# Performance work log

Hardware: AMD Instinct MI355X
Metric: run time of the kernel (lower is better)

## Reference

```python
import jax, jax.numpy as jnp
import numpy as np

B = 4096       # batch
N_IN = 784     # input neurons
BANKS = 64     # banks per layer
L = 16         # layers of banks (layer 0 = input banks)
FAN = 8        # fan-out per source bank into next layer
D = 10         # n_neurons_per_hidd_bank
N_CONN = (L - 1) * BANKS * FAN  # total bank connections (7680)


def setup_inputs() -> dict:
    key = jax.random.key(0)
    ks = jax.random.split(key, 7)
    x = jax.random.normal(ks[0], (B, N_IN), jnp.float32)
    # input2hidden: Linear(N_IN, D, bias=True) for each input bank -> weight [D, N_IN]
    Wi = jax.random.normal(ks[1], (BANKS, D, N_IN), jnp.float32) / np.sqrt(N_IN).astype(np.float32)
    bi = jax.random.normal(ks[2], (BANKS, D), jnp.float32) * 0.1
    # per-edge gate: Linear(D, 1, bias=True); bias shifted so gates are a mix of open/closed
    Wg = jax.random.normal(ks[3], (L - 1, BANKS, FAN, D), jnp.float32) / np.sqrt(D).astype(np.float32)
    bg = jax.random.normal(ks[4], (L - 1, BANKS, FAN), jnp.float32) * 0.3 + 0.2
    # per-edge data: Linear(D, D, bias=False) -> weight [out=D, in=D]
    Wd = jax.random.normal(ks[5], (L - 1, BANKS, FAN, D, D), jnp.float32) / np.sqrt(D).astype(np.float32)
    # hidden2output: Linear(D, 1, bias=False) per output bank
    Wo = jax.random.normal(ks[6], (BANKS, D), jnp.float32) / np.sqrt(D).astype(np.float32)
    return {"x": x, "Wi": Wi, "bi": bi, "Wg": Wg, "bg": bg, "Wd": Wd, "Wo": Wo}


def reference(x, Wi, bi, Wg, bg, Wd, Wo):
    # forward_softgate with defaults: no batch norm, dropout p=0 (identity),
    # gates enabled (b_no_gates=False), positive gate loss, no gate_status.
    batch = x.shape[0]
    # static scatter targets: source bank s feeds banks (s+k)%BANKS of next layer
    s = np.arange(BANKS)[:, None]
    k = np.arange(FAN)[None, :]
    tgt = jnp.asarray(((s + k) % BANKS).reshape(-1))  # [BANKS*FAN]

    # input banks (layer 0); the target loop applies ReLU to every bank, incl. input banks
    acts = jax.nn.relu(jnp.einsum('bi,koi->bko', x, Wi) + bi)  # [B, BANKS, D]

    def layer(acts, w):
        wg, bgl, wd = w
        # gate: hardtanh(Linear(acts), 0, 1) per edge -> [B, BANKS, FAN]
        gate = jnp.clip(jnp.einsum('bsd,skd->bsk', acts, wg) + bgl, 0.0, 1.0)
        # data: Linear(D, D, bias=False); torch y = x @ W.T with W[out, in]
        data = jnp.einsum('bsd,sked->bske', acts, wd)  # [B, BANKS, FAN, D]
        contrib = (gate[..., None] * data).reshape(batch, BANKS * FAN, D)
        acc = jnp.zeros_like(acts).at[:, tgt].add(contrib)  # scatter-add into target banks
        new_acts = jax.nn.relu(acc)
        gate_sum = gate.sum(axis=(1, 2))                   # per-sample gate activity
        n_open = (gate > 0.0).sum().astype(jnp.float32)    # open-gate count
        return new_acts, (gate_sum, n_open)

    acts, (gate_sums, n_opens) = jax.lax.scan(layer, acts, (Wg, bg, Wd))
    total_gate_act = (gate_sums.sum(axis=0) / N_CONN)[:, None]          # [B, 1]
    prob_open_gate = n_opens.sum() / (N_CONN * batch)                   # scalar
    # output banks = last layer banks, Linear(D,1,bias=False) each, then ReLU
    output = jax.nn.relu(jnp.einsum('bkd,kd->bk', acts, Wo))            # [B, BANKS]
    return output, total_gate_act, prob_open_gate
```

## Files before the change

### kernel.cpp

```cpp
#include <hip/hip_runtime.h>
#include <type_traits>

#define NIN 784
#define BANKS 64
#define NLAYER 15
#define FAN 8
#define DD 10
#define NBF 640
#define NSW 4
#define NSB 8

typedef float f32x2 __attribute__((ext_vector_type(2)));

__device__ __forceinline__ float f4c_rt(const float4& v, int c) {
    return c == 0 ? v.x : (c == 1 ? v.y : (c == 2 ? v.z : v.w));
}

typedef const __attribute__((address_space(1))) void gas_void;
typedef __attribute__((address_space(3))) void las_void;

__device__ __forceinline__ void gll16(const void* g, void* l) {
    __builtin_amdgcn_global_load_lds((gas_void*)g, (las_void*)l, 16, 0, 0);
}

#define NCH (NLAYER*FAN*28*64)
#define NBI (NLAYER*2*64)
#define GEMM_BLKS 640
#define TR_BLKS   848

__global__ __launch_bounds__(256)
void fused_prologue(const float* __restrict__ x, const float* __restrict__ Wi,
                    const float* __restrict__ bi,
                    const float* __restrict__ Wg, const float* __restrict__ bg,
                    const float* __restrict__ Wd,
                    float* __restrict__ acts,
                    float4* __restrict__ chunk_t, float4* __restrict__ bias_t)
{
    if (blockIdx.x >= GEMM_BLKS) {
        int tid = (blockIdx.x - GEMM_BLKS) * 256 + threadIdx.x;
        if (tid < NCH) {
            int b = tid & 63;
            int rk = tid >> 6;
            int r = rk % 28;
            int lk = rk / 28;
            int k = lk & 7;
            int l = lk >> 3;
            float4 v;
            if (r < 25) {
                v = ((const float4*)Wd)[(((size_t)(l*64+b)*8 + k)*25) + r];
            } else {
                int q = r - 25;
                size_t base = ((size_t)(l*64+b)*8 + k)*10 + 4*q;
                float t[4];
#pragma unroll
                for (int c = 0; c < 4; ++c)
                    t[c] = (4*q + c < 10) ? Wg[base + c] : 0.f;
                v = make_float4(t[0], t[1], t[2], t[3]);
            }
            chunk_t[tid] = v;
        } else if (tid < NCH + NBI) {
            int t2 = tid - NCH;
            int b = t2 & 63;
            int q = (t2 >> 6) & 1;
            int l = t2 >> 7;
            bias_t[t2] = ((const float4*)bg)[(size_t)(l*64+b)*2 + q];
        }
        return;
    }

    __shared__ float As[16][68];
    __shared__ float Bs[16][68];
    const int tid = threadIdx.x;
    const int tx = tid & 15, ty = tid >> 4;
    const int m0 = (blockIdx.x & 63) * 64;
    const int n0 = (blockIdx.x >> 6) * 64;

    float acc[4][4];
#pragma unroll
    for (int i = 0; i < 4; ++i)
#pragma unroll
        for (int j = 0; j < 4; ++j) acc[i][j] = 0.f;

    for (int kb = 0; kb < NIN / 16; ++kb) {
        {
            int m = tid >> 2, kq = tid & 3;
            float4 v = *(const float4*)(x + (m0 + m) * NIN + kb * 16 + kq * 4);
            As[kq*4+0][m] = v.x; As[kq*4+1][m] = v.y;
            As[kq*4+2][m] = v.z; As[kq*4+3][m] = v.w;
            float4 u = *(const float4*)(Wi + (n0 + m) * NIN + kb * 16 + kq * 4);
            Bs[kq*4+0][m] = u.x; Bs[kq*4+1][m] = u.y;
            Bs[kq*4+2][m] = u.z; Bs[kq*4+3][m] = u.w;
        }
        __syncthreads();
#pragma unroll
        for (int k = 0; k < 16; ++k) {
            float4 a4 = *(const float4*)(&As[k][ty*4]);
            float4 b4 = *(const float4*)(&Bs[k][tx*4]);
            float av[4] = {a4.x, a4.y, a4.z, a4.w};
            float bv[4] = {b4.x, b4.y, b4.z, b4.w};
#pragma unroll
            for (int i = 0; i < 4; ++i)
#pragma unroll
                for (int j = 0; j < 4; ++j)
                    acc[i][j] = fmaf(av[i], bv[j], acc[i][j]);
        }
        __syncthreads();
    }
    float4 bv = *(const float4*)(bi + n0 + tx*4);
#pragma unroll
    for (int i = 0; i < 4; ++i) {
        int row = m0 + ty*4 + i;
        float4 o;
        o.x = fmaxf(acc[i][0] + bv.x, 0.f);
        o.y = fmaxf(acc[i][1] + bv.y, 0.f);
        o.z = fmaxf(acc[i][2] + bv.z, 0.f);
        o.w = fmaxf(acc[i][3] + bv.w, 0.f);
        *(float4*)(acts + row * NBF + n0 + tx*4) = o;
    }
}

__global__ __launch_bounds__(256, 2)
void routenet_v10(const float* __restrict__ acts0,
                  const float4* __restrict__ chunk_t, const float4* __restrict__ bias_t,
                  const float* __restrict__ Wo,
                  float* __restrict__ out, unsigned int* __restrict__ nopen_g)
{
    __shared__ float4 wdstage[2][28][64];
    __shared__ float  exH1[2][NSW][5][64];
    __shared__ float  exH0[2][NSW][5][64];

    const int tid  = threadIdx.x;
    const int lane = tid & 63;
    const int w    = tid >> 6;
    const int g    = w & 1;
    const int h    = w >> 1;
    const int b0   = blockIdx.x * NSB + g * NSW;

    f32x2 A2[2][DD];
#pragma unroll
    for (int p = 0; p < 2; ++p) {
        const float2* q0 = (const float2*)(acts0 + (size_t)(b0 + 2*p    ) * NBF + lane * DD);
        const float2* q1 = (const float2*)(acts0 + (size_t)(b0 + 2*p + 1) * NBF + lane * DD);
#pragma unroll
        for (int d2 = 0; d2 < 5; ++d2) {
            float2 v0 = q0[d2], v1 = q1[d2];
            A2[p][2*d2  ] = f32x2{v0.x, v1.x};
            A2[p][2*d2+1] = f32x2{v0.y, v1.y};
        }
    }

    f32x2 gs2[2] = { f32x2{0.f,0.f}, f32x2{0.f,0.f} };
    unsigned int nop = 0;

    auto stage_chunk = [&](int l, int k, int pdst) {
        const float4* base = chunk_t + (size_t)(l*8 + k) * 28 * 64;
#pragma unroll
        for (int j = 0; j < 7; ++j) {
            int r = w + 4 * j;
            gll16(base + r*64 + lane, &wdstage[pdst][r][0]);
        }
    };

    stage_chunk(0, 0, 0);
    float4 bq0 = bias_t[lane];
    float4 bq1 = bias_t[64 + lane];
    asm volatile("s_waitcnt vmcnt(0)" ::: "memory");
    asm volatile("s_barrier" ::: "memory");

    for (int l = 0; l < NLAYER; ++l) {
        float4 bn0 = bq0, bn1 = bq1;
        if (l + 1 < NLAYER) {
            bn0 = bias_t[(size_t)((l+1)*2    ) * 64 + lane];
            bn1 = bias_t[(size_t)((l+1)*2 + 1) * 64 + lane];
        }

        f32x2 acc2[2][5];
#pragma unroll
        for (int p = 0; p < 2; ++p)
#pragma unroll
            for (int el = 0; el < 5; ++el) acc2[p][el] = f32x2{0.f, 0.f};

        auto chunk_body = [&](auto Hc, int k, int p) {
            constexpr int H = Hc.value;
            float4 wgq[3];
#pragma unroll
            for (int q = 0; q < 3; ++q) wgq[q] = wdstage[p][25 + q][lane];
            const float bias = f4c_rt((k & 4) ? bq1 : bq0, k & 3);
            float wgv[DD];
#pragma unroll
            for (int d = 0; d < DD; ++d) wgv[d] = f4c_rt(wgq[d >> 2], d & 3);

            f32x2 gz[2];
#pragma unroll
            for (int pp = 0; pp < 2; ++pp) {
                f32x2 z = f32x2{bias, bias};
#pragma unroll
                for (int d = 0; d < DD; ++d)
                    z = __builtin_elementwise_fma(A2[pp][d], f32x2{wgv[d], wgv[d]}, z);
                f32x2 gate = __builtin_elementwise_min(
                                 __builtin_elementwise_max(z, f32x2{0.f, 0.f}),
                                 f32x2{1.f, 1.f});
                if (H == 0) {
                    gs2[pp] += gate;
                    nop += (z[0] > 0.f) ? 1u : 0u;
                    nop += (z[1] > 0.f) ? 1u : 0u;
                }
                gz[pp] = gate;
            }

            float4 wv[13];
#pragma unroll
            for (int i = 0; i < 13; ++i) wv[i] = wdstage[p][12*H + i][lane];

            const int src = (lane - k) & 63;
#pragma unroll
            for (int el = 0; el < 5; ++el) {
#pragma unroll
                for (int pp = 0; pp < 2; ++pp) {
                    f32x2 dot = f32x2{0.f, 0.f};
#pragma unroll
                    for (int d = 0; d < DD; ++d) {
                        const int idx = (5*H + el) * 10 + d - 48*H;
                        const float wd = f4c_rt(wv[idx >> 2], idx & 3);
                        dot = __builtin_elementwise_fma(A2[pp][d], f32x2{wd, wd}, dot);
                    }
                    f32x2 cc = gz[pp] * dot;
                    f32x2 r;
                    r[0] = __shfl(cc[0], src, 64);
                    r[1] = __shfl(cc[1], src, 64);
                    acc2[pp][el] += r;
                }
            }
        };

#pragma unroll
        for (int c = 0; c < 8; ++c) {
            const int p = c & 1;
            if (c < 7) {
                stage_chunk(l, c + 1, p ^ 1);
                asm volatile("s_waitcnt vmcnt(7)" ::: "memory");
            } else if (l + 1 < NLAYER) {
                stage_chunk(l + 1, 0, p ^ 1);
                asm volatile("s_waitcnt vmcnt(7)" ::: "memory");
            } else {
                asm volatile("s_waitcnt vmcnt(0)" ::: "memory");
            }
            if (c == 0) {
                asm volatile("s_waitcnt lgkmcnt(0)" ::: "memory");
            }
            asm volatile("s_barrier" ::: "memory");

            __builtin_amdgcn_s_setprio(1);
            if (c == 0 && l > 0 && h == 1) {
#pragma unroll
                for (int s = 0; s < NSW; ++s)
#pragma unroll
                    for (int el = 0; el < 5; ++el)
                        A2[s>>1][el][s&1] = exH0[g][s][el][lane];
            }
            if (h == 0) chunk_body(std::integral_constant<int,0>{}, c, p);
            else        chunk_body(std::integral_constant<int,1>{}, c, p);
            __builtin_amdgcn_s_setprio(0);

            if (c < 7) {
                asm volatile("s_waitcnt lgkmcnt(0)" ::: "memory");
                asm volatile("s_barrier" ::: "memory");
            }
        }

        if (h == 0) {
#pragma unroll
            for (int s = 0; s < NSW; ++s)
#pragma unroll
                for (int el = 0; el < 5; ++el)
                    A2[s>>1][el][s&1] = fmaxf(acc2[s>>1][el][s&1], 0.f);
        } else {
#pragma unroll
            for (int s = 0; s < NSW; ++s)
#pragma unroll
                for (int el = 0; el < 5; ++el) {
                    float v = fmaxf(acc2[s>>1][el][s&1], 0.f);
                    A2[s>>1][5 + el][s&1] = v;
                    exH1[g][s][el][lane] = v;
                }
        }
        asm volatile("s_waitcnt lgkmcnt(0)" ::: "memory");
        asm volatile("s_barrier" ::: "memory");

        if (h == 0) {
#pragma unroll
            for (int s = 0; s < NSW; ++s)
#pragma unroll
                for (int el = 0; el < 5; ++el)
                    A2[s>>1][5 + el][s&1] = exH1[g][s][el][lane];
            if (l + 1 < NLAYER) {
#pragma unroll
                for (int s = 0; s < NSW; ++s)
#pragma unroll
                    for (int el = 0; el < 5; ++el)
                        exH0[g][s][el][lane] = A2[s>>1][el][s&1];
            }
        }
        bq0 = bn0; bq1 = bn1;
    }

    if (h == 0) {
        float wo[DD];
        const float2* pw = (const float2*)(Wo + lane * DD);
#pragma unroll
        for (int d2 = 0; d2 < 5; ++d2) {
            float2 v = pw[d2];
            wo[2*d2] = v.x; wo[2*d2+1] = v.y;
        }
#pragma unroll
        for (int p = 0; p < 2; ++p) {
            f32x2 o = f32x2{0.f, 0.f};
#pragma unroll
            for (int d = 0; d < DD; ++d)
                o = __builtin_elementwise_fma(A2[p][d], f32x2{wo[d], wo[d]}, o);
            out[(size_t)(b0 + 2*p    ) * BANKS + lane] = fmaxf(o[0], 0.f);
            out[(size_t)(b0 + 2*p + 1) * BANKS + lane] = fmaxf(o[1], 0.f);
        }

#pragma unroll
        for (int s = 0; s < NSW; ++s) {
            float v = gs2[s>>1][s&1];
#pragma unroll
            for (int off = 32; off; off >>= 1) v += __shfl_xor(v, off, 64);
            if (lane == 0)
                out[(size_t)4096 * BANKS + b0 + s] = v * (1.0f / 7680.0f);
        }
        {
            unsigned int v = nop;
#pragma unroll
            for (int off = 32; off; off >>= 1) v += __shfl_xor(v, off, 64);
            if (lane == 0) atomicAdd(nopen_g, v);
        }
    }
}

__global__ __launch_bounds__(256, 2)
void routenet_v5f(const float* __restrict__ acts0,
                  const float* __restrict__ x, const float* __restrict__ Wi,
                  const float* __restrict__ bi,
                  const float* __restrict__ Wg, const float* __restrict__ bg,
                  const float* __restrict__ Wd, const float* __restrict__ Wo,
                  float* __restrict__ out, unsigned int* __restrict__ nopen_g)
{
    __shared__ float4 wdstage[2][28][64];
    __shared__ float4 biasbuf[2][2][64];
    __shared__ float  exch[2][NSW][5][64];

    const int tid  = threadIdx.x;
    const int lane = tid & 63;
    const int w    = tid >> 6;
    const int g    = w & 1;
    const int h    = w >> 1;
    const int b0   = blockIdx.x * NSB + g * NSW;

    float a[NSW][DD];

    if (acts0) {
#pragma unroll
        for (int s = 0; s < NSW; ++s) {
            const float2* p = (const float2*)(acts0 + (size_t)(b0 + s) * NBF + lane * DD);
#pragma unroll
            for (int d2 = 0; d2 < 5; ++d2) {
                float2 v = p[d2];
                a[s][d2*2]   = v.x;
                a[s][d2*2+1] = v.y;
            }
        }
    } else {
        for (int s = 0; s < NSW; ++s) {
            const float* xb2 = x + (size_t)(b0 + s) * NIN;
            for (int d = 0; d < DD; ++d) {
                int n = lane * DD + d;
                const float* wr = Wi + (size_t)n * NIN;
                float z = bi[n];
                for (int i = 0; i < NIN; ++i) z = fmaf(xb2[i], wr[i], z);
                a[s][d] = fmaxf(z, 0.f);
            }
        }
    }

    float gsum[NSW];
#pragma unroll
    for (int s = 0; s < NSW; ++s) gsum[s] = 0.f;
    unsigned int nop = 0;

    auto stage_chunk = [&](int l, int k, int pdst) {
        const float* wd_base = Wd + (size_t)l * (BANKS*FAN*DD*DD)
                                  + (size_t)lane * (FAN*DD*DD) + k * (DD*DD);
        const float* wg_base = Wg + (size_t)l * (BANKS*FAN*DD)
                                  + lane * (FAN*DD) + ((10*k) >> 2) * 4;
#pragma unroll
        for (int j = 0; j < 7; ++j) {
            int r = w + 4 * j;
            if (r < 25) gll16(wd_base + r * 4, &wdstage[pdst][r][0]);
            else        gll16(wg_base + (r - 25) * 4, &wdstage[pdst][r][0]);
        }
    };
    auto stage_bias = [&](int l) {
        int q = w & 1;
        gll16(bg + (size_t)l * (BANKS*FAN) + lane * FAN + q * 4,
              &biasbuf[l & 1][q][0]);
    };

    stage_chunk(0, 0, 0);
    stage_bias(0);
    asm volatile("s_waitcnt vmcnt(0)" ::: "memory");
    asm volatile("s_barrier" ::: "memory");

    for (int l = 0; l < NLAYER; ++l) {
        const int lp = l & 1;
        float acc[NSW][5];
#pragma unroll
        for (int s = 0; s < NSW; ++s)
#pragma unroll
            for (int el = 0; el < 5; ++el) acc[s][el] = 0.f;

        auto chunk_body = [&](auto Hc, int k, int p) {
            constexpr int H = Hc.value;
            float4 wgq[3];
#pragma unroll
            for (int q = 0; q < 3; ++q) wgq[q] = wdstage[p][25 + q][lane];
            const float bias = f4c_rt(biasbuf[lp][(k >> 2) & 1][lane], k & 3);
            float wgv[DD];
            if ((k & 1) == 0) {
#pragma unroll
                for (int d = 0; d < DD; ++d) wgv[d] = f4c_rt(wgq[d >> 2], d & 3);
            } else {
#pragma unroll
                for (int d = 0; d < DD; ++d) wgv[d] = f4c_rt(wgq[(d+2) >> 2], (d+2) & 3);
            }

            float gz[NSW];
#pragma unroll
            for (int s = 0; s < NSW; ++s) {
                float z = bias;
#pragma unroll
                for (int d = 0; d < DD; ++d) z = fmaf(a[s][d], wgv[d], z);
                float gate = fminf(fmaxf(z, 0.f), 1.f);
                if (H == 0) { gsum[s] += gate; nop += (z > 0.f) ? 1u : 0u; }
                gz[s] = gate;
            }

            float4 wv[13];
#pragma unroll
            for (int i = 0; i < 13; ++i) wv[i] = wdstage[p][12*H + i][lane];

            const int src = (lane - k) & 63;
#pragma unroll
            for (int el = 0; el < 5; ++el) {
#pragma unroll
                for (int s = 0; s < NSW; ++s) {
                    float dot = 0.f;
#pragma unroll
                    for (int d = 0; d < DD; ++d) {
                        const int idx = (5*H + el) * 10 + d - 48*H;
                        dot = fmaf(a[s][d], f4c_rt(wv[idx >> 2], idx & 3), dot);
                    }
                    acc[s][el] += __shfl(gz[s] * dot, src, 64);
                }
            }
        };

#pragma unroll
        for (int c = 0; c < 8; ++c) {
            const int p = c & 1;
            if (c < 7) {
                stage_chunk(l, c + 1, p ^ 1);
                asm volatile("s_waitcnt vmcnt(7)" ::: "memory");
            } else if (l + 1 < NLAYER) {
                stage_chunk(l + 1, 0, p ^ 1);
                stage_bias(l + 1);
                asm volatile("s_waitcnt vmcnt(8)" ::: "memory");
            } else {
                asm volatile("s_waitcnt vmcnt(0)" ::: "memory");
            }
            asm volatile("s_barrier" ::: "memory");

            if (h == 0) chunk_body(std::integral_constant<int,0>{}, c, p);
            else        chunk_body(std::integral_constant<int,1>{}, c, p);

            if (c < 7) {
                asm volatile("s_waitcnt lgkmcnt(0)" ::: "memory");
                asm volatile("s_barrier" ::: "memory");
            }
        }

        if (h == 0) {
#pragma unroll
            for (int s = 0; s < NSW; ++s)
#pragma unroll
                for (int el = 0; el < 5; ++el)
                    a[s][el] = fmaxf(acc[s][el], 0.f);
        } else {
#pragma unroll
            for (int s = 0; s < NSW; ++s)
#pragma unroll
                for (int el = 0; el < 5; ++el) {
                    a[s][5 + el] = fmaxf(acc[s][el], 0.f);
                    exch[g][s][el][lane] = a[s][5 + el];
                }
        }
        asm volatile("s_waitcnt lgkmcnt(0)" ::: "memory");
        asm volatile("s_barrier" ::: "memory");

        if (h == 0) {
#pragma unroll
            for (int s = 0; s < NSW; ++s)
#pragma unroll
                for (int el = 0; el < 5; ++el)
                    a[s][5 + el] = exch[g][s][el][lane];
            if (l + 1 < NLAYER) {
#pragma unroll
                for (int s = 0; s < NSW; ++s)
#pragma unroll
                    for (int el = 0; el < 5; ++el)
                        exch[g][s][el][lane] = a[s][el];
            }
        }
        if (l + 1 < NLAYER) {
            asm volatile("s_waitcnt lgkmcnt(0)" ::: "memory");
            asm volatile("s_barrier" ::: "memory");
            if (h == 1) {
#pragma unroll
                for (int s = 0; s < NSW; ++s)
#pragma unroll
                    for (int el = 0; el < 5; ++el)
                        a[s][el] = exch[g][s][el][lane];
            }
        }
    }

    if (h == 0) {
        float wo[DD];
        const float2* p = (const float2*)(Wo + lane * DD);
#pragma unroll
        for (int d2 = 0; d2 < 5; ++d2) {
            float2 v = p[d2];
            wo[d2*2] = v.x; wo[d2*2+1] = v.y;
        }
#pragma unroll
        for (int s = 0; s < NSW; ++s) {
            float v = 0.f;
#pragma unroll
            for (int d = 0; d < DD; ++d) v = fmaf(a[s][d], wo[d], v);
            out[(size_t)(b0 + s) * BANKS + lane] = fmaxf(v, 0.f);
        }

#pragma unroll
        for (int s = 0; s < NSW; ++s) {
            float v = gsum[s];
#pragma unroll
            for (int off = 32; off; off >>= 1) v += __shfl_xor(v, off, 64);
            if (lane == 0)
                out[(size_t)4096 * BANKS + b0 + s] = v * (1.0f / 7680.0f);
        }
        {
            unsigned int v = nop;
#pragma unroll
            for (int off = 32; off; off >>= 1) v += __shfl_xor(v, off, 64);
            if (lane == 0) atomicAdd(nopen_g, v);
        }
    }
}

__global__ void finalize_prob(const unsigned int* __restrict__ nopen,
                              float* __restrict__ out)
{
    out[4096*64 + 4096] = (float)(*nopen) / 31457280.0f;
}

extern "C" void kernel_launch(void* const* d_in, const int* in_sizes, int n_in,
                              void* d_out, int out_size, void* d_ws, size_t ws_size,
                              hipStream_t stream)
{
    const float* x  = (const float*)d_in[0];
    const float* Wi = (const float*)d_in[1];
    const float* bi = (const float*)d_in[2];
    const float* Wg = (const float*)d_in[3];
    const float* bg = (const float*)d_in[4];
    const float* Wd = (const float*)d_in[5];
    const float* Wo = (const float*)d_in[6];
    float* out = (float*)d_out;

    const size_t ACTS_BYTES  = (size_t)4096 * NBF * 4;
    const size_t CHUNK_BYTES = (size_t)NCH * 16;
    const size_t BIAS_BYTES  = (size_t)NBI * 16;
    const size_t FULL_BYTES  = ACTS_BYTES + CHUNK_BYTES + BIAS_BYTES + 64;

    bool full    = ws_size >= FULL_BYTES;
    bool actonly = !full && ws_size >= ACTS_BYTES + 64;

    float* acts0 = (full || actonly) ? (float*)d_ws : nullptr;
    float4* chunk_t = full ? (float4*)((char*)d_ws + ACTS_BYTES) : nullptr;
    float4* bias_t  = full ? (float4*)((char*)d_ws + ACTS_BYTES + CHUNK_BYTES) : nullptr;
    unsigned int* nopen = full
        ? (unsigned int*)((char*)d_ws + ACTS_BYTES + CHUNK_BYTES + BIAS_BYTES)
        : (actonly ? (unsigned int*)((char*)d_ws + ACTS_BYTES)
                   : (unsigned int*)d_ws);

    hipMemsetAsync(nopen, 0, 4, stream);

    if (full) {
        fused_prologue<<<GEMM_BLKS + TR_BLKS, 256, 0, stream>>>(
            x, Wi, bi, Wg, bg, Wd, acts0, chunk_t, bias_t);
        routenet_v10<<<4096 / NSB, 256, 0, stream>>>(
            acts0, chunk_t, bias_t, Wo, out, nopen);
    } else {
        if (acts0) {
            fused_prologue<<<GEMM_BLKS, 256, 0, stream>>>(
                x, Wi, bi, Wg, bg, Wd, acts0, nullptr, nullptr);
        }
        routenet_v5f<<<4096 / NSB, 256, 0, stream>>>(
            acts0, x, Wi, bi, Wg, bg, Wd, Wo, out, nopen);
    }
    finalize_prob<<<1, 1, 0, stream>>>(nopen, out);
}
```

Measured before the change: 281.2 us.

## Split output neurons across four waves per 4-sample block, stage bias via LDS

Each block now processes 4 samples with all four waves sharing them, each wave computing a quarter of the output-neuron slice (3/3/2/2 elements), instead of two sample groups each split into two halves. The grid doubles to 1024 blocks. A single LDS exchange per layer broadcasts the new activations to every wave. Bias is staged into LDS with async loads instead of register prefetch, and the nopen memset is folded into the prologue kernel to drop a launch. The trade-off is that every wave recomputes all gates redundantly, which adds ALU work per sample in exchange for more parallelism and fewer barriers.

```diff
diff --git a/kernel.cpp b/kernel.cpp
--- a/kernel.cpp
+++ b/kernel.cpp
@@ -8,7 +8,7 @@
 #define DD 10
 #define NBF 640
 #define NSW 4
-#define NSB 8
+#define NSB_V5 8
 
 typedef float f32x2 __attribute__((ext_vector_type(2)));
 
@@ -34,9 +34,11 @@
                     const float* __restrict__ Wg, const float* __restrict__ bg,
                     const float* __restrict__ Wd,
                     float* __restrict__ acts,
-                    float4* __restrict__ chunk_t, float4* __restrict__ bias_t)
+                    float4* __restrict__ chunk_t, float4* __restrict__ bias_t,
+                    unsigned int* __restrict__ nopen)
 {
     if (blockIdx.x >= GEMM_BLKS) {
+        if (blockIdx.x == GEMM_BLKS && threadIdx.x == 0 && nopen) *nopen = 0u;
         int tid = (blockIdx.x - GEMM_BLKS) * 256 + threadIdx.x;
         if (tid < NCH) {
             int b = tid & 63;
@@ -120,21 +122,19 @@
 }
 
 __global__ __launch_bounds__(256, 2)
-void routenet_v10(const float* __restrict__ acts0,
+void routenet_v12(const float* __restrict__ acts0,
                   const float4* __restrict__ chunk_t, const float4* __restrict__ bias_t,
                   const float* __restrict__ Wo,
                   float* __restrict__ out, unsigned int* __restrict__ nopen_g)
 {
     __shared__ float4 wdstage[2][28][64];
-    __shared__ float  exH1[2][NSW][5][64];
-    __shared__ float  exH0[2][NSW][5][64];
+    __shared__ float4 biasbuf[2][2][64];
+    __shared__ float  exch[NSW][DD][64];
 
     const int tid  = threadIdx.x;
     const int lane = tid & 63;
     const int w    = tid >> 6;
-    const int g    = w & 1;
-    const int h    = w >> 1;
-    const int b0   = blockIdx.x * NSB + g * NSW;
+    const int b0   = blockIdx.x * NSW;
 
     f32x2 A2[2][DD];
 #pragma unroll
@@ -160,32 +160,35 @@
             gll16(base + r*64 + lane, &wdstage[pdst][r][0]);
         }
     };
+    auto stage_bias = [&](int l) {
+        int q = w & 1;
+        gll16(bias_t + (size_t)(l*2 + q)*64 + lane, &biasbuf[l & 1][q][0]);
+    };
 
     stage_chunk(0, 0, 0);
-    float4 bq0 = bias_t[lane];
-    float4 bq1 = bias_t[64 + lane];
+    stage_bias(0);
     asm volatile("s_waitcnt vmcnt(0)" ::: "memory");
     asm volatile("s_barrier" ::: "memory");
 
     for (int l = 0; l < NLAYER; ++l) {
-        float4 bn0 = bq0, bn1 = bq1;
-        if (l + 1 < NLAYER) {
-            bn0 = bias_t[(size_t)((l+1)*2    ) * 64 + lane];
-            bn1 = bias_t[(size_t)((l+1)*2 + 1) * 64 + lane];
-        }
-
-        f32x2 acc2[2][5];
+        const int lp = l & 1;
+        f32x2 acc2[2][3];
 #pragma unroll
         for (int p = 0; p < 2; ++p)
 #pragma unroll
-            for (int el = 0; el < 5; ++el) acc2[p][el] = f32x2{0.f, 0.f};
-
-        auto chunk_body = [&](auto Hc, int k, int p) {
-            constexpr int H = Hc.value;
+            for (int e = 0; e < 3; ++e) acc2[p][e] = f32x2{0.f, 0.f};
+
+        auto chunk_body = [&](auto Qc, int k, int p) {
+            constexpr int Q   = Qc.value;
+            constexpr int el0 = (Q==0) ? 0 : (Q==1) ? 3 : (Q==2) ? 6 : 8;
+            constexpr int nel = (Q < 2) ? 3 : 2;
+            constexpr int qd0 = (Q==0) ? 0 : (Q==1) ? 7 : (Q==2) ? 15 : 20;
+            constexpr int nq  = (Q < 2) ? 8 : 5;
+
             float4 wgq[3];
 #pragma unroll
             for (int q = 0; q < 3; ++q) wgq[q] = wdstage[p][25 + q][lane];
-            const float bias = f4c_rt((k & 4) ? bq1 : bq0, k & 3);
+            const float bias = f4c_rt(biasbuf[lp][(k >> 2) & 1][lane], k & 3);
             float wgv[DD];
 #pragma unroll
             for (int d = 0; d < DD; ++d) wgv[d] = f4c_rt(wgq[d >> 2], d & 3);
@@ -200,7 +203,7 @@
                 f32x2 gate = __builtin_elementwise_min(
                                  __builtin_elementwise_max(z, f32x2{0.f, 0.f}),
                                  f32x2{1.f, 1.f});
-                if (H == 0) {
+                if (Q == 0) {
                     gs2[pp] += gate;
                     nop += (z[0] > 0.f) ? 1u : 0u;
                     nop += (z[1] > 0.f) ? 1u : 0u;
@@ -208,260 +211,28 @@
                 gz[pp] = gate;
             }
 
-            float4 wv[13];
-#pragma unroll
-            for (int i = 0; i < 13; ++i) wv[i] = wdstage[p][12*H + i][lane];
+            float4 wv[8];
+#pragma unroll
+            for (int i = 0; i < nq; ++i) wv[i] = wdstage[p][qd0 + i][lane];
 
             const int src = (lane - k) & 63;
 #pragma unroll
-            for (int el = 0; el < 5; ++el) {
+            for (int e = 0; e < nel; ++e) {
+                const int el = el0 + e;
 #pragma unroll
                 for (int pp = 0; pp < 2; ++pp) {
                     f32x2 dot = f32x2{0.f, 0.f};
 #pragma unroll
                     for (int d = 0; d < DD; ++d) {
-                        const int idx = (5*H + el) * 10 + d - 48*H;
-                        const float wd = f4c_rt(wv[idx >> 2], idx & 3);
+                        const int idx = el * 10 + d;
+                        const float wd = f4c_rt(wv[idx/4 - qd0], idx & 3);
                         dot = __builtin_elementwise_fma(A2[pp][d], f32x2{wd, wd}, dot);
                     }
                     f32x2 cc = gz[pp] * dot;
                     f32x2 r;
                     r[0] = __shfl(cc[0], src, 64);
                     r[1] = __shfl(cc[1], src, 64);
-                    acc2[pp][el] += r;
-                }
-            }
-        };
-
-#pragma unroll
-        for (int c = 0; c < 8; ++c) {
-            const int p = c & 1;
-            if (c < 7) {
-                stage_chunk(l, c + 1, p ^ 1);
-                asm volatile("s_waitcnt vmcnt(7)" ::: "memory");
-            } else if (l + 1 < NLAYER) {
-                stage_chunk(l + 1, 0, p ^ 1);
-                asm volatile("s_waitcnt vmcnt(7)" ::: "memory");
-            } else {
-                asm volatile("s_waitcnt vmcnt(0)" ::: "memory");
-            }
-            if (c == 0) {
-                asm volatile("s_waitcnt lgkmcnt(0)" ::: "memory");
-            }
-            asm volatile("s_barrier" ::: "memory");
-
-            __builtin_amdgcn_s_setprio(1);
-            if (c == 0 && l > 0 && h == 1) {
-#pragma unroll
-                for (int s = 0; s < NSW; ++s)
-#pragma unroll
-                    for (int el = 0; el < 5; ++el)
-                        A2[s>>1][el][s&1] = exH0[g][s][el][lane];
-            }
-            if (h == 0) chunk_body(std::integral_constant<int,0>{}, c, p);
-            else        chunk_body(std::integral_constant<int,1>{}, c, p);
-            __builtin_amdgcn_s_setprio(0);
-
-            if (c < 7) {
-                asm volatile("s_waitcnt lgkmcnt(0)" ::: "memory");
-                asm volatile("s_barrier" ::: "memory");
-            }
-        }
-
-        if (h == 0) {
-#pragma unroll
-            for (int s = 0; s < NSW; ++s)
-#pragma unroll
-                for (int el = 0; el < 5; ++el)
-                    A2[s>>1][el][s&1] = fmaxf(acc2[s>>1][el][s&1], 0.f);
-        } else {
-#pragma unroll
-            for (int s = 0; s < NSW; ++s)
-#pragma unroll
-                for (int el = 0; el < 5; ++el) {
-                    float v = fmaxf(acc2[s>>1][el][s&1], 0.f);
-                    A2[s>>1][5 + el][s&1] = v;
-                    exH1[g][s][el][lane] = v;
-                }
-        }
-        asm volatile("s_waitcnt lgkmcnt(0)" ::: "memory");
-        asm volatile("s_barrier" ::: "memory");
-
-        if (h == 0) {
-#pragma unroll
-            for (int s = 0; s < NSW; ++s)
-#pragma unroll
-                for (int el = 0; el < 5; ++el)
-                    A2[s>>1][5 + el][s&1] = exH1[g][s][el][lane];
-            if (l + 1 < NLAYER) {
-#pragma unroll
-                for (int s = 0; s < NSW; ++s)
-#pragma unroll
-                    for (int el = 0; el < 5; ++el)
-                        exH0[g][s][el][lane] = A2[s>>1][el][s&1];
-            }
-        }
-        bq0 = bn0; bq1 = bn1;
-    }
-
-    if (h == 0) {
-        float wo[DD];
-        const float2* pw = (const float2*)(Wo + lane * DD);
-#pragma unroll
-        for (int d2 = 0; d2 < 5; ++d2) {
-            float2 v = pw[d2];
-            wo[2*d2] = v.x; wo[2*d2+1] = v.y;
-        }
-#pragma unroll
-        for (int p = 0; p < 2; ++p) {
-            f32x2 o = f32x2{0.f, 0.f};
-#pragma unroll
-            for (int d = 0; d < DD; ++d)
-                o = __builtin_elementwise_fma(A2[p][d], f32x2{wo[d], wo[d]}, o);
-            out[(size_t)(b0 + 2*p    ) * BANKS + lane] = fmaxf(o[0], 0.f);
-            out[(size_t)(b0 + 2*p + 1) * BANKS + lane] = fmaxf(o[1], 0.f);
-        }
-
-#pragma unroll
-        for (int s = 0; s < NSW; ++s) {
-            float v = gs2[s>>1][s&1];
-#pragma unroll
-            for (int off = 32; off; off >>= 1) v += __shfl_xor(v, off, 64);
-            if (lane == 0)
-                out[(size_t)4096 * BANKS + b0 + s] = v * (1.0f / 7680.0f);
-        }
-        {
-            unsigned int v = nop;
-#pragma unroll
-            for (int off = 32; off; off >>= 1) v += __shfl_xor(v, off, 64);
-            if (lane == 0) atomicAdd(nopen_g, v);
-        }
-    }
-}
-
-__global__ __launch_bounds__(256, 2)
-void routenet_v5f(const float* __restrict__ acts0,
-                  const float* __restrict__ x, const float* __restrict__ Wi,
-                  const float* __restrict__ bi,
-                  const float* __restrict__ Wg, const float* __restrict__ bg,
-                  const float* __restrict__ Wd, const float* __restrict__ Wo,
-                  float* __restrict__ out, unsigned int* __restrict__ nopen_g)
-{
-    __shared__ float4 wdstage[2][28][64];
-    __shared__ float4 biasbuf[2][2][64];
-    __shared__ float  exch[2][NSW][5][64];
-
-    const int tid  = threadIdx.x;
-    const int lane = tid & 63;
-    const int w    = tid >> 6;
-    const int g    = w & 1;
-    const int h    = w >> 1;
-    const int b0   = blockIdx.x * NSB + g * NSW;
-
-    float a[NSW][DD];
-
-    if (acts0) {
-#pragma unroll
-        for (int s = 0; s < NSW; ++s) {
-            const float2* p = (const float2*)(acts0 + (size_t)(b0 + s) * NBF + lane * DD);
-#pragma unroll
-            for (int d2 = 0; d2 < 5; ++d2) {
-                float2 v = p[d2];
-                a[s][d2*2]   = v.x;
-                a[s][d2*2+1] = v.y;
-            }
-        }
-    } else {
-        for (int s = 0; s < NSW; ++s) {
-            const float* xb2 = x + (size_t)(b0 + s) * NIN;
-            for (int d = 0; d < DD; ++d) {
-                int n = lane * DD + d;
-                const float* wr = Wi + (size_t)n * NIN;
-                float z = bi[n];
-                for (int i = 0; i < NIN; ++i) z = fmaf(xb2[i], wr[i], z);
-                a[s][d] = fmaxf(z, 0.f);
-            }
-        }
-    }
-
-    float gsum[NSW];
-#pragma unroll
-    for (int s = 0; s < NSW; ++s) gsum[s] = 0.f;
-    unsigned int nop = 0;
-
-    auto stage_chunk = [&](int l, int k, int pdst) {
-        const float* wd_base = Wd + (size_t)l * (BANKS*FAN*DD*DD)
-                                  + (size_t)lane * (FAN*DD*DD) + k * (DD*DD);
-        const float* wg_base = Wg + (size_t)l * (BANKS*FAN*DD)
-                                  + lane * (FAN*DD) + ((10*k) >> 2) * 4;
-#pragma unroll
-        for (int j = 0; j < 7; ++j) {
-            int r = w + 4 * j;
-            if (r < 25) gll16(wd_base + r * 4, &wdstage[pdst][r][0]);
-            else        gll16(wg_base + (r - 25) * 4, &wdstage[pdst][r][0]);
-        }
-    };
-    auto stage_bias = [&](int l) {
-        int q = w & 1;
-        gll16(bg + (size_t)l * (BANKS*FAN) + lane * FAN + q * 4,
-              &biasbuf[l & 1][q][0]);
-    };
-
-    stage_chunk(0, 0, 0);
-    stage_bias(0);
-    asm volatile("s_waitcnt vmcnt(0)" ::: "memory");
-    asm volatile("s_barrier" ::: "memory");
-
-    for (int l = 0; l < NLAYER; ++l) {
-        const int lp = l & 1;
-        float acc[NSW][5];
-#pragma unroll
-        for (int s = 0; s < NSW; ++s)
-#pragma unroll
-            for (int el = 0; el < 5; ++el) acc[s][el] = 0.f;
-
-        auto chunk_body = [&](auto Hc, int k, int p) {
-            constexpr int H = Hc.value;
-            float4 wgq[3];
-#pragma unroll
-            for (int q = 0; q < 3; ++q) wgq[q] = wdstage[p][25 + q][lane];
-            const float bias = f4c_rt(biasbuf[lp][(k >> 2) & 1][lane], k & 3);
-            float wgv[DD];
-            if ((k & 1) == 0) {
-#pragma unroll
-                for (int d = 0; d < DD; ++d) wgv[d] = f4c_rt(wgq[d >> 2], d & 3);
-            } else {
-#pragma unroll
-                for (int d = 0; d < DD; ++d) wgv[d] = f4c_rt(wgq[(d+2) >> 2], (d+2) & 3);
-            }
-
-            float gz[NSW];
-#pragma unroll
-            for (int s = 0; s < NSW; ++s) {
-                float z = bias;
-#pragma unroll
-                for (int d = 0; d < DD; ++d) z = fmaf(a[s][d], wgv[d], z);
-                float gate = fminf(fmaxf(z, 0.f), 1.f);
-                if (H == 0) { gsum[s] += gate; nop += (z > 0.f) ? 1u : 0u; }
-                gz[s] = gate;
-            }
-
-            float4 wv[13];
-#pragma unroll
-            for (int i = 0; i < 13; ++i) wv[i] = wdstage[p][12*H + i][lane];
-
-            const int src = (lane - k) & 63;
-#pragma unroll
-            for (int el = 0; el < 5; ++el) {
-#pragma unroll
-                for (int s = 0; s < NSW; ++s) {
-                    float dot = 0.f;
-#pragma unroll
-                    for (int d = 0; d < DD; ++d) {
-                        const int idx = (5*H + el) * 10 + d - 48*H;
-                        dot = fmaf(a[s][d], f4c_rt(wv[idx >> 2], idx & 3), dot);
-                    }
-                    acc[s][el] += __shfl(gz[s] * dot, src, 64);
+                    acc2[pp][e] += r;
                 }
             }
         };
@@ -481,8 +252,10 @@
             }
             asm volatile("s_barrier" ::: "memory");
 
-            if (h == 0) chunk_body(std::integral_constant<int,0>{}, c, p);
-            else        chunk_body(std::integral_constant<int,1>{}, c, p);
+            if      (w == 0) chunk_body(std::integral_constant<int,0>{}, c, p);
+            else if (w == 1) chunk_body(std::integral_constant<int,1>{}, c, p);
+            else if (w == 2) chunk_body(std::integral_constant<int,2>{}, c, p);
+            else             chunk_body(std::integral_constant<int,3>{}, c, p);
 
             if (c < 7) {
                 asm volatile("s_waitcnt lgkmcnt(0)" ::: "memory");
@@ -490,15 +263,231 @@
             }
         }
 
+        {
+            const int el0 = (w==0) ? 0 : (w==1) ? 3 : (w==2) ? 6 : 8;
+            const int nel = (w < 2) ? 3 : 2;
+#pragma unroll
+            for (int s = 0; s < NSW; ++s)
+#pragma unroll
+                for (int e = 0; e < 3; ++e) {
+                    if (e < nel) {
+                        float v = fmaxf(acc2[s>>1][e][s&1], 0.f);
+                        A2[s>>1][el0 + e][s&1] = v;
+                        exch[s][el0 + e][lane] = v;
+                    }
+                }
+        }
+        asm volatile("s_waitcnt lgkmcnt(0)" ::: "memory");
+        asm volatile("s_barrier" ::: "memory");
+        {
+            const int el0 = (w==0) ? 0 : (w==1) ? 3 : (w==2) ? 6 : 8;
+            const int nel = (w < 2) ? 3 : 2;
+#pragma unroll
+            for (int el = 0; el < DD; ++el) {
+                if (el < el0 || el >= el0 + nel) {
+#pragma unroll
+                    for (int s = 0; s < NSW; ++s)
+                        A2[s>>1][el][s&1] = exch[s][el][lane];
+                }
+            }
+        }
+    }
+
+    if (w == 0) {
+        float wo[DD];
+        const float2* pw = (const float2*)(Wo + lane * DD);
+#pragma unroll
+        for (int d2 = 0; d2 < 5; ++d2) {
+            float2 v = pw[d2];
+            wo[2*d2] = v.x; wo[2*d2+1] = v.y;
+        }
+#pragma unroll
+        for (int p = 0; p < 2; ++p) {
+            f32x2 o = f32x2{0.f, 0.f};
+#pragma unroll
+            for (int d = 0; d < DD; ++d)
+                o = __builtin_elementwise_fma(A2[p][d], f32x2{wo[d], wo[d]}, o);
+            out[(size_t)(b0 + 2*p    ) * BANKS + lane] = fmaxf(o[0], 0.f);
+            out[(size_t)(b0 + 2*p + 1) * BANKS + lane] = fmaxf(o[1], 0.f);
+        }
+
+#pragma unroll
+        for (int s = 0; s < NSW; ++s) {
+            float v = gs2[s>>1][s&1];
+#pragma unroll
+            for (int off = 32; off; off >>= 1) v += __shfl_xor(v, off, 64);
+            if (lane == 0)
+                out[(size_t)4096 * BANKS + b0 + s] = v * (1.0f / 7680.0f);
+        }
+        {
+            unsigned int v = nop;
+#pragma unroll
+            for (int off = 32; off; off >>= 1) v += __shfl_xor(v, off, 64);
+            if (lane == 0) atomicAdd(nopen_g, v);
+        }
+    }
+}
+
+__global__ __launch_bounds__(256, 2)
+void routenet_v5f(const float* __restrict__ acts0,
+                  const float* __restrict__ x, const float* __restrict__ Wi,
+                  const float* __restrict__ bi,
+                  const float* __restrict__ Wg, const float* __restrict__ bg,
+                  const float* __restrict__ Wd, const float* __restrict__ Wo,
+                  float* __restrict__ out, unsigned int* __restrict__ nopen_g)
+{
+    __shared__ float4 wdstage[2][28][64];
+    __shared__ float4 biasbuf[2][2][64];
+    __shared__ float  exch[2][4][5][64];
+
+    const int tid  = threadIdx.x;
+    const int lane = tid & 63;
+    const int w    = tid >> 6;
+    const int g    = w & 1;
+    const int h    = w >> 1;
+    const int b0   = blockIdx.x * NSB_V5 + g * 4;
+
+    float a[4][DD];
+
+    if (acts0) {
+#pragma unroll
+        for (int s = 0; s < 4; ++s) {
+            const float2* p = (const float2*)(acts0 + (size_t)(b0 + s) * NBF + lane * DD);
+#pragma unroll
+            for (int d2 = 0; d2 < 5; ++d2) {
+                float2 v = p[d2];
+                a[s][d2*2]   = v.x;
+                a[s][d2*2+1] = v.y;
+            }
+        }
+    } else {
+        for (int s = 0; s < 4; ++s) {
+            const float* xb2 = x + (size_t)(b0 + s) * NIN;
+            for (int d = 0; d < DD; ++d) {
+                int n = lane * DD + d;
+                const float* wr = Wi + (size_t)n * NIN;
+                float z = bi[n];
+                for (int i = 0; i < NIN; ++i) z = fmaf(xb2[i], wr[i], z);
+                a[s][d] = fmaxf(z, 0.f);
+            }
+        }
+    }
+
+    float gsum[4];
+#pragma unroll
+    for (int s = 0; s < 4; ++s) gsum[s] = 0.f;
+    unsigned int nop = 0;
+
+    auto stage_chunk = [&](int l, int k, int pdst) {
+        const float* wd_base = Wd + (size_t)l * (BANKS*FAN*DD*DD)
+                                  + (size_t)lane * (FAN*DD*DD) + k * (DD*DD);
+        const float* wg_base = Wg + (size_t)l * (BANKS*FAN*DD)
+                                  + lane * (FAN*DD) + ((10*k) >> 2) * 4;
+#pragma unroll
+        for (int j = 0; j < 7; ++j) {
+            int r = w + 4 * j;
+            if (r < 25) gll16(wd_base + r * 4, &wdstage[pdst][r][0]);
+            else        gll16(wg_base + (r - 25) * 4, &wdstage[pdst][r][0]);
+        }
+    };
+    auto stage_bias = [&](int l) {
+        int q = w & 1;
+        gll16(bg + (size_t)l * (BANKS*FAN) + lane * FAN + q * 4,
+              &biasbuf[l & 1][q][0]);
+    };
+
+    stage_chunk(0, 0, 0);
+    stage_bias(0);
+    asm volatile("s_waitcnt vmcnt(0)" ::: "memory");
+    asm volatile("s_barrier" ::: "memory");
+
+    for (int l = 0; l < NLAYER; ++l) {
+        const int lp = l & 1;
+        float acc[4][5];
+#pragma unroll
+        for (int s = 0; s < 4; ++s)
+#pragma unroll
+            for (int el = 0; el < 5; ++el) acc[s][el] = 0.f;
+
+        auto chunk_body = [&](auto Hc, int k, int p) {
+            constexpr int H = Hc.value;
+            float4 wgq[3];
+#pragma unroll
+            for (int q = 0; q < 3; ++q) wgq[q] = wdstage[p][25 + q][lane];
+            const float bias = f4c_rt(biasbuf[lp][(k >> 2) & 1][lane], k & 3);
+            float wgv[DD];
+            if ((k & 1) == 0) {
+#pragma unroll
+                for (int d = 0; d < DD; ++d) wgv[d] = f4c_rt(wgq[d >> 2], d & 3);
+            } else {
+#pragma unroll
+                for (int d = 0; d < DD; ++d) wgv[d] = f4c_rt(wgq[(d+2) >> 2], (d+2) & 3);
+            }
+
+            float gz[4];
+#pragma unroll
+            for (int s = 0; s < 4; ++s) {
+                float z = bias;
+#pragma unroll
+                for (int d = 0; d < DD; ++d) z = fmaf(a[s][d], wgv[d], z);
+                float gate = fminf(fmaxf(z, 0.f), 1.f);
+                if (H == 0) { gsum[s] += gate; nop += (z > 0.f) ? 1u : 0u; }
+                gz[s] = gate;
+            }
+
+            float4 wv[13];
+#pragma unroll
+            for (int i = 0; i < 13; ++i) wv[i] = wdstage[p][12*H + i][lane];
+
+            const int src = (lane - k) & 63;
+#pragma unroll
+            for (int el = 0; el < 5; ++el) {
+#pragma unroll
+                for (int s = 0; s < 4; ++s) {
+                    float dot = 0.f;
+#pragma unroll
+                    for (int d = 0; d < DD; ++d) {
+                        const int idx = (5*H + el) * 10 + d - 48*H;
+                        dot = fmaf(a[s][d], f4c_rt(wv[idx >> 2], idx & 3), dot);
+                    }
+                    acc[s][el] += __shfl(gz[s] * dot, src, 64);
+                }
+            }
+        };
+
+#pragma unroll
+        for (int c = 0; c < 8; ++c) {
+            const int p = c & 1;
+            if (c < 7) {
+                stage_chunk(l, c + 1, p ^ 1);
+                asm volatile("s_waitcnt vmcnt(7)" ::: "memory");
+            } else if (l + 1 < NLAYER) {
+                stage_chunk(l + 1, 0, p ^ 1);
+                stage_bias(l + 1);
+                asm volatile("s_waitcnt vmcnt(8)" ::: "memory");
+            } else {
+                asm volatile("s_waitcnt vmcnt(0)" ::: "memory");
+            }
+            asm volatile("s_barrier" ::: "memory");
+
+            if (h == 0) chunk_body(std::integral_constant<int,0>{}, c, p);
+            else        chunk_body(std::integral_constant<int,1>{}, c, p);
+
+            if (c < 7) {
+                asm volatile("s_waitcnt lgkmcnt(0)" ::: "memory");
+                asm volatile("s_barrier" ::: "memory");
+            }
+        }
+
         if (h == 0) {
 #pragma unroll
-            for (int s = 0; s < NSW; ++s)
+            for (int s = 0; s < 4; ++s)
 #pragma unroll
                 for (int el = 0; el < 5; ++el)
                     a[s][el] = fmaxf(acc[s][el], 0.f);
         } else {
 #pragma unroll
-            for (int s = 0; s < NSW; ++s)
+            for (int s = 0; s < 4; ++s)
 #pragma unroll
                 for (int el = 0; el < 5; ++el) {
                     a[s][5 + el] = fmaxf(acc[s][el], 0.f);
@@ -510,13 +499,13 @@
 
         if (h == 0) {
 #pragma unroll
-            for (int s = 0; s < NSW; ++s)
+            for (int s = 0; s < 4; ++s)
 #pragma unroll
                 for (int el = 0; el < 5; ++el)
                     a[s][5 + el] = exch[g][s][el][lane];
             if (l + 1 < NLAYER) {
 #pragma unroll
-                for (int s = 0; s < NSW; ++s)
+                for (int s = 0; s < 4; ++s)
 #pragma unroll
                     for (int el = 0; el < 5; ++el)
                         exch[g][s][el][lane] = a[s][el];
@@ -527,7 +516,7 @@
             asm volatile("s_barrier" ::: "memory");
             if (h == 1) {
 #pragma unroll
-                for (int s = 0; s < NSW; ++s)
+                for (int s = 0; s < 4; ++s)
 #pragma unroll
                     for (int el = 0; el < 5; ++el)
                         a[s][el] = exch[g][s][el][lane];
@@ -544,7 +533,7 @@
             wo[d2*2] = v.x; wo[d2*2+1] = v.y;
         }
 #pragma unroll
-        for (int s = 0; s < NSW; ++s) {
+        for (int s = 0; s < 4; ++s) {
             float v = 0.f;
 #pragma unroll
             for (int d = 0; d < DD; ++d) v = fmaf(a[s][d], wo[d], v);
@@ -552,7 +541,7 @@
         }
 
 #pragma unroll
-        for (int s = 0; s < NSW; ++s) {
+        for (int s = 0; s < 4; ++s) {
             float v = gsum[s];
 #pragma unroll
             for (int off = 32; off; off >>= 1) v += __shfl_xor(v, off, 64);
@@ -603,19 +592,18 @@
         : (actonly ? (unsigned int*)((char*)d_ws + ACTS_BYTES)
                    : (unsigned int*)d_ws);
 
-    hipMemsetAsync(nopen, 0, 4, stream);
-
     if (full) {
         fused_prologue<<<GEMM_BLKS + TR_BLKS, 256, 0, stream>>>(
-            x, Wi, bi, Wg, bg, Wd, acts0, chunk_t, bias_t);
-        routenet_v10<<<4096 / NSB, 256, 0, stream>>>(
+            x, Wi, bi, Wg, bg, Wd, acts0, chunk_t, bias_t, nopen);
+        routenet_v12<<<4096 / NSW, 256, 0, stream>>>(
             acts0, chunk_t, bias_t, Wo, out, nopen);
     } else {
+        hipMemsetAsync(nopen, 0, 4, stream);
         if (acts0) {
             fused_prologue<<<GEMM_BLKS, 256, 0, stream>>>(
-                x, Wi, bi, Wg, bg, Wd, acts0, nullptr, nullptr);
-        }
-        routenet_v5f<<<4096 / NSB, 256, 0, stream>>>(
+                x, Wi, bi, Wg, bg, Wd, acts0, nullptr, nullptr, nullptr);
+        }
+        routenet_v5f<<<4096 / NSB_V5, 256, 0, stream>>>(
             acts0, x, Wi, bi, Wg, bg, Wd, Wo, out, nopen);
     }
     finalize_prob<<<1, 1, 0, stream>>>(nopen, out);
```

After: 421.4 us. 49.9% more time.
